# Performance work log

Hardware: AMD Instinct MI355X
Metric: run time of the kernel (lower is better)

## Reference

```python
import jax, jax.numpy as jnp
import numpy as np

# dims
B, L, HID = 4, 4096, 1024
H, D = 16, 64            # num_mem_heads, head_dim = HID // H
DM = 128                 # mem_intermediate = head_dim * mem_expansion_factor (2.0)
K = 4                    # conv_kernel
CS = 64                  # chunk_size
EPS = 1e-6


def setup_inputs() -> dict:
    key = jax.random.key(0)
    ks = jax.random.split(key, 16)
    std = 0.02
    f = lambda i, shape: jax.random.normal(ks[i], shape, jnp.float32) * std
    return {
        'hidden_states': jax.random.normal(ks[0], (B, L, HID), jnp.float32),
        'Wq': f(1, (HID, HID)), 'Wk': f(2, (HID, HID)), 'Wv': f(3, (HID, HID)),
        'conv_q_w': f(4, (HID, K)), 'conv_q_b': jnp.zeros((HID,), jnp.float32),
        'conv_k_w': f(5, (HID, K)), 'conv_k_b': jnp.zeros((HID,), jnp.float32),
        'conv_v_w': f(6, (HID, K)), 'conv_v_b': jnp.zeros((HID,), jnp.float32),
        'q_norm_w': jnp.ones((D,), jnp.float32), 'k_norm_w': jnp.ones((D,), jnp.float32),
        'mem_decay_w': f(7, (H, HID)), 'mem_decay_b': jnp.zeros((H,), jnp.float32),
        'surprise_w': f(8, (H, HID)), 'surprise_b': jnp.zeros((H,), jnp.float32),
        'lr_w': f(9, (H, HID)), 'lr_b': jnp.zeros((H,), jnp.float32),
        'W1': f(10, (H, D, DM)), 'W2': f(11, (H, DM, D)),
    }


def _silu_bwd(x):
    sig = jax.nn.sigmoid(x)
    return sig + jax.nn.silu(x) * (1.0 - sig)


def _rmsnorm(x, w):
    xf = x.astype(jnp.float32)
    var = jnp.mean(xf * xf, axis=-1, keepdims=True)
    return w * (xf * jax.lax.rsqrt(var + EPS)).astype(x.dtype)


def _causal_conv_silu(x, w, b):
    # x: [B, L, H, D] -> depthwise causal conv over time on C=H*D channels -> [B, H, L, D]
    Bs, Ls, Hh, Dd = x.shape
    xc = jnp.swapaxes(x.reshape(Bs, Ls, Hh * Dd), 1, 2)        # [B, C, L]
    xp = jnp.pad(xc, ((0, 0), (0, 0), (K - 1, 0)))             # left pad -> causal
    y = b[None, :, None]
    for k in range(K):
        y = y + w[None, :, k:k + 1] * xp[:, :, k:k + Ls]
    y = jax.nn.silu(y)
    return jnp.swapaxes(y.reshape(Bs, Hh, Dd, Ls), -2, -1)     # [B, H, L, D]


def _decayed_scan(d, v, init):
    # y_t = d_t * y_{t-1} + v_t, y_0 = init; d: [B,H,C,1], v: [B,H,C,dim], init: [B,H,1,dim]
    def comb(x, y):
        a1, b1 = x
        a2, b2 = y
        return a1 * a2, b1 * a2 + b2
    A, Bv = jax.lax.associative_scan(comb, (d, v), axis=2)
    return A * init + Bv


def _forward(hidden_states, Wq, Wk, Wv, conv_q_w, conv_q_b, conv_k_w, conv_k_b,
             conv_v_w, conv_v_b, q_norm_w, k_norm_w, mem_decay_w, mem_decay_b,
             surprise_w, surprise_b, lr_w, lr_b, W1, W2):
    x = hidden_states
    # projections -> [B, L, H, D]
    q = (x @ Wq.T).reshape(B, L, H, D)
    k = (x @ Wk.T).reshape(B, L, H, D)
    v = (x @ Wv.T).reshape(B, L, H, D)
    # depthwise causal conv + silu -> [B, H, L, D]
    q = _causal_conv_silu(q, conv_q_w, conv_q_b)
    k = _causal_conv_silu(k, conv_k_w, conv_k_b)
    v = _causal_conv_silu(v, conv_v_w, conv_v_b)
    # QK RMSNorm (per head_dim)
    q = _rmsnorm(q, q_norm_w)
    k = _rmsnorm(k, k_norm_w)
    # per-timestep gates -> [B, H, L, 1]
    mem_decay = 1.0 - jax.nn.sigmoid(x @ mem_decay_w.T + mem_decay_b)
    surprise_decay = jax.nn.sigmoid(x @ surprise_w.T + surprise_b)
    lr = jax.nn.sigmoid(x @ lr_w.T + lr_b)
    to_gate = lambda g: jnp.swapaxes(g, -2, -1)[..., None]
    mem_decay, surprise_decay, lr = to_gate(mem_decay), to_gate(surprise_decay), to_gate(lr)

    # split sequence into chunks: [N, B, H, CS, *]
    N = L // CS
    ch = lambda t: jnp.moveaxis(t.reshape(B, H, N, CS, t.shape[-1]), 2, 0)
    qs, ks_, vs = ch(q), ch(k), ch(v)
    mds, sds, lrs = ch(mem_decay), ch(surprise_decay), ch(lr)

    W1b = jnp.broadcast_to(W1[None], (B, H, D, DM))
    W2b = jnp.broadcast_to(W2[None], (B, H, DM, D))
    carry0 = (W1b, W2b,
              jnp.zeros((B, H, 1, DM), jnp.float32),   # W1_surprise
              jnp.zeros((B, H, 1, D), jnp.float32),    # W2_surprise
              jnp.zeros((B, H, 1, D), jnp.float32),    # key_momentum
              jnp.zeros((B, H, 1, DM), jnp.float32))   # X1_momentum

    def step(carry, inp):
        W1c, W2c, W1s, W2s, kmom, xmom = carry
        qc, kc, vc, md, sd, lrc = inp
        # memory MLP fwd with chunk-frozen weights
        Z1 = kc @ W1c                       # [B,H,CS,DM]
        X1 = jax.nn.silu(Z1)
        mems = X1 @ W2c                     # [B,H,CS,D]
        g_m = mems - vc
        g_Z1 = (g_m @ jnp.swapaxes(W2c, -2, -1)) * _silu_bwd(Z1)
        g_m = -lrc * g_m
        g_Z1 = -lrc * g_Z1
        # activation-space surprise/momentum scans (decayed linear recurrence)
        W1s_n = _decayed_scan(sd, g_Z1, W1s)[:, :, -1:, :]
        W2s_n = _decayed_scan(sd, g_m, W2s)[:, :, -1:, :]
        kmom_n = _decayed_scan(md, kc, kmom)[:, :, -1:, :]
        xmom_n = _decayed_scan(md, X1, xmom)[:, :, -1:, :]
        # weight update at chunk boundary: decay + outer-product of accumulated factors
        mprod = jnp.prod(md, axis=2, keepdims=True)          # [B,H,1,1]
        W1n = mprod * W1c + jnp.swapaxes(kmom_n, -2, -1) @ W1s_n
        W2n = mprod * W2c + jnp.swapaxes(xmom_n, -2, -1) @ W2s_n
        # retrieve with updated memory
        y = jax.nn.silu(qc @ W1n) @ W2n                      # [B,H,CS,D]
        return (W1n, W2n, W1s_n, W2s_n, kmom_n, xmom_n), y

    _, ys = jax.lax.scan(step, carry0, (qs, ks_, vs, mds, sds, lrs))
    mem_states = jnp.moveaxis(ys, 0, 2).reshape(B, H, L, D)
    # replicate torch: mem_states.transpose(-2,-1).reshape(B, L, H*D)
    return jnp.swapaxes(mem_states, -2, -1).reshape(B, L, H * D)


def reference(hidden_states, Wq, Wk, Wv, conv_q_w, conv_q_b, conv_k_w, conv_k_b,
              conv_v_w, conv_v_b, q_norm_w, k_norm_w, mem_decay_w, mem_decay_b,
              surprise_w, surprise_b, lr_w, lr_b, W1, W2):
    return _forward(hidden_states, Wq, Wk, Wv, conv_q_w, conv_q_b, conv_k_w, conv_k_b,
                    conv_v_w, conv_v_b, q_norm_w, k_norm_w, mem_decay_w, mem_decay_b,
                    surprise_w, surprise_b, lr_w, lr_b, W1, W2)
```

## Files before the change

kernel.cpp:

```cpp
#include <hip/hip_runtime.h>

#define B_ 4
#define L_ 4096
#define HID_ 1024
#define H_ 16
#define D_ 64
#define DM_ 128
#define CS_ 64
#define NCH_ 64
#define EPS_ 1e-6f

typedef __attribute__((ext_vector_type(8))) short bfrag_t;
typedef __attribute__((ext_vector_type(4))) float facc_t;

#define MFMA16(a,b,c) __builtin_amdgcn_mfma_f32_16x16x32_bf16(a,b,c,0,0,0)

__device__ __forceinline__ float sigf(float x){ return 1.0f/(1.0f + __expf(-x)); }

__device__ __forceinline__ unsigned f2bfu(float x){
  unsigned u = __float_as_uint(x);
  return (u + 0x7fffu + ((u>>16)&1u)) >> 16;
}
__device__ __forceinline__ float bf2f(unsigned short s){
  return __uint_as_float(((unsigned)s)<<16);
}
__device__ __forceinline__ unsigned cvtpk(float lo, float hi){
  unsigned r;
  asm("v_cvt_pk_bf16_f32 %0, %1, %2" : "=v"(r) : "v"(lo), "v"(hi));
  return r;
}
__device__ __forceinline__ float bflo(unsigned u){ return __uint_as_float(u<<16); }
__device__ __forceinline__ float bfhi(unsigned u){ return __uint_as_float(u & 0xffff0000u); }

__device__ __forceinline__ void gld16(const unsigned short* g, unsigned short* l){
  __builtin_amdgcn_global_load_lds(
      (const __attribute__((address_space(1))) unsigned int*)(const void*)g,
      (__attribute__((address_space(3))) unsigned int*)(void*)l,
      16, 0, 0);
}

#define DPP_ADD_(x, ctrl) x += __int_as_float(__builtin_amdgcn_update_dpp(0, __float_as_int(x), ctrl, 0xf, 0xf, true))
__device__ __forceinline__ float wsum64(float x){
  DPP_ADD_(x, 0x111);
  DPP_ADD_(x, 0x112);
  DPP_ADD_(x, 0x114);
  DPP_ADD_(x, 0x118);
  const float a = __int_as_float(__builtin_amdgcn_readlane(__float_as_int(x), 15));
  const float b = __int_as_float(__builtin_amdgcn_readlane(__float_as_int(x), 31));
  const float c = __int_as_float(__builtin_amdgcn_readlane(__float_as_int(x), 47));
  const float d = __int_as_float(__builtin_amdgcn_readlane(__float_as_int(x), 63));
  return (a+b)+(c+d);
}

__global__ __launch_bounds__(256) void cast_kernel(
    const float* __restrict__ x,  const float* __restrict__ wq,
    const float* __restrict__ wk, const float* __restrict__ wv,
    unsigned short* __restrict__ xb,  unsigned short* __restrict__ wqb,
    unsigned short* __restrict__ wkb, unsigned short* __restrict__ wvb)
{
  const int bid = blockIdx.x;
  const float* s; unsigned short* d; int base;
  if (bid < 16384){ s = x; d = xb; base = bid*1024; }
  else {
    int r = bid - 16384; const int a = r >> 10; r &= 1023; base = r*1024;
    s = (a==0)?wq:(a==1)?wk:wv;
    d = (a==0)?wqb:(a==1)?wkb:wvb;
  }
  const int i = base + threadIdx.x*4;
  float4 v = *(const float4*)(s + i);
  unsigned lo = f2bfu(v.x) | (f2bfu(v.y)<<16);
  unsigned hi = f2bfu(v.z) | (f2bfu(v.w)<<16);
  uint2 o; o.x = lo; o.y = hi;
  *(uint2*)(d + i) = o;
}

__global__ __launch_bounds__(256, 2) void gemm_bf16_nt(
    const unsigned short* __restrict__ A, const unsigned short* __restrict__ Bw,
    unsigned short* __restrict__ C, int M, int N, int K)
{
  __shared__ __align__(16) unsigned short As[2][4096];
  __shared__ __align__(16) unsigned short Bs[2][4096];
  const int tid = threadIdx.x;
  const int lane = tid & 63, wave = tid >> 6;
  const int lq = lane & 15, quad = lane >> 4;
  const int m0 = blockIdx.y*128, n0 = blockIdx.x*128;
  const int row = tid >> 2, ks = (tid & 3)*8;
  const int mo = (wave & 1)*64, no = (wave >> 1)*64;

  const unsigned short* pa0 = A  + (size_t)(m0 + row)*K + ks;
  const unsigned short* pa1 = pa0 + (size_t)64*K;
  const unsigned short* pb0 = Bw + (size_t)(n0 + row)*K + ks;
  const unsigned short* pb1 = pb0 + (size_t)64*K;

  facc_t acc[4][4];
  #pragma unroll
  for (int i=0;i<4;++i)
    #pragma unroll
    for (int j=0;j<4;++j) acc[i][j] = (facc_t){0.f,0.f,0.f,0.f};

  auto stage = [&](int buf, int kt){
    const int off = kt*32;
    unsigned short* ab = &As[buf][wave*512];
    unsigned short* bb = &Bs[buf][wave*512];
    gld16(pa0 + off, ab);
    gld16(pa1 + off, ab + 2048);
    gld16(pb0 + off, bb);
    gld16(pb1 + off, bb + 2048);
  };

  const int kiters = K >> 5;
  stage(0, 0);
  __syncthreads();

  int cur = 0;
  for (int kt = 0; kt < kiters; ++kt){
    if (kt+1 < kiters) stage(cur^1, kt+1);
    bfrag_t af[4], bf[4];
    #pragma unroll
    for (int mt=0;mt<4;++mt) af[mt] = *(const bfrag_t*)&As[cur][(mo+mt*16+lq)*32 + quad*8];
    #pragma unroll
    for (int nt=0;nt<4;++nt) bf[nt] = *(const bfrag_t*)&Bs[cur][(no+nt*16+lq)*32 + quad*8];
    #pragma unroll
    for (int mt=0;mt<4;++mt)
      #pragma unroll
      for (int nt=0;nt<4;++nt)
        acc[mt][nt] = MFMA16(af[mt], bf[nt], acc[mt][nt]);
    __syncthreads();
    cur ^= 1;
  }

  #pragma unroll
  for (int mt=0;mt<4;++mt)
    #pragma unroll
    for (int nt=0;nt<4;++nt)
      #pragma unroll
      for (int r=0;r<4;++r){
        const int rr = m0 + mo + mt*16 + quad*4 + r;
        const int cc = n0 + no + nt*16 + lq;
        const int t = cc >> 10, hh = (cc >> 6) & 15, dd = cc & 63;
        const int b = rr >> 12, l = rr & 4095;
        C[((((size_t)t*B_ + b)*H_ + hh)*L_ + l)*64 + dd]
            = (unsigned short)f2bfu(acc[mt][nt][r]);
      }
}

__global__ __launch_bounds__(256, 2) void gates_kernel(
  const float* __restrict__ x,
  const float* __restrict__ mdw, const float* __restrict__ mdb,
  const float* __restrict__ sw,  const float* __restrict__ sb,
  const float* __restrict__ lw,  const float* __restrict__ lb,
  float* __restrict__ cmb, float* __restrict__ c1b, float* __restrict__ ppb)
{
  __shared__ float xs[64][68];
  __shared__ float wg[48][68];
  const int tid = threadIdx.x;
  const int m0 = blockIdx.x * 64;
  const int tx = tid & 15, ty = tid >> 4;
  float acc[4][3];
  #pragma unroll
  for (int r=0;r<4;++r){ acc[r][0]=0.f; acc[r][1]=0.f; acc[r][2]=0.f; }

  for (int k0 = 0; k0 < HID_; k0 += 64){
    {
      const int r = tid >> 2, kq = tid & 3;
      const float* xp = x + (size_t)(m0 + r) * HID_ + k0 + kq*16;
      #pragma unroll
      for (int u=0;u<4;++u){
        float4 v = *(const float4*)(xp + u*4);
        *(float4*)&xs[r][kq*16 + u*4] = v;
      }
    }
    #pragma unroll
    for (int u=0;u<3;++u){
      const int idx = tid + 256*u;
      const int gi = idx >> 4, q = idx & 15;
      const float* wp = (gi < 16) ? (mdw + (size_t)gi*HID_)
                      : (gi < 32) ? (sw  + (size_t)(gi-16)*HID_)
                                  : (lw  + (size_t)(gi-32)*HID_);
      float4 v = *(const float4*)(wp + k0 + q*4);
      *(float4*)&wg[gi][q*4] = v;
    }
    __syncthreads();
    for (int kk=0; kk<64; ++kk){
      float xv[4], wv[3];
      #pragma unroll
      for (int r=0;r<4;++r) xv[r] = xs[ty*4+r][kk];
      #pragma unroll
      for (int gg=0;gg<3;++gg) wv[gg] = wg[tx*3+gg][kk];
      #pragma unroll
      for (int r=0;r<4;++r)
        #pragma unroll
        for (int gg=0;gg<3;++gg) acc[r][gg] += xv[r]*wv[gg];
    }
    __syncthreads();
  }

  float (*ls)[68] = xs;
  #pragma unroll
  for (int gg=0; gg<3; ++gg){
    const int gi = tx*3 + gg;
    const int s = gi >> 4, hh = gi & 15;
    const float bias = (s==0) ? mdb[hh] : (s==1) ? sb[hh] : lb[hh];
    #pragma unroll
    for (int r=0;r<4;++r) ls[gi][ty*4+r] = acc[r][gg] + bias;
  }
  __syncthreads();

  const int lane = tid & 63, wv2 = tid >> 6;
  const int b = m0 >> 12, n = (m0 & 4095) >> 6;
  #pragma unroll
  for (int u=0;u<4;++u){
    const int hh = wv2*4 + u;
    const float md = 1.0f - sigf(ls[hh][lane]);
    const float sd = sigf(ls[16+hh][lane]);
    const float lr = sigf(ls[32+hh][lane]);
    float vm = md, vs = sd;
    #pragma unroll
    for (int off = 1; off < 64; off <<= 1){
      float om = __shfl_down(vm, off);
      float os = __shfl_down(vs, off);
      if (lane + off < 64){ vm *= om; vs *= os; }
    }
    float mex = __shfl_down(vm, 1);
    float sex = __shfl_down(vs, 1);
    if (lane == 63){ mex = 1.0f; sex = 1.0f; }
    const size_t base = ((size_t)(b*16 + hh)*NCH_ + n)*64;
    cmb[base + lane] = mex;
    c1b[base + lane] = -lr * sex;
    if (lane == 0){
      ppb[((size_t)(b*16+hh)*NCH_ + n)*2 + 0] = vm;
      ppb[((size_t)(b*16+hh)*NCH_ + n)*2 + 1] = vs;
    }
  }
}

#define HALO_T_ ((size_t)64*64*3*64)

__global__ __launch_bounds__(192) void halo_kernel(
  const unsigned short* __restrict__ qg, const unsigned short* __restrict__ kg,
  const unsigned short* __restrict__ vg, unsigned short* __restrict__ halo)
{
  const int blk = blockIdx.x;
  const int bh = blk / 63;
  const int ch = blk % 63 + 1;
  const int tid = threadIdx.x;
  const int tt = tid >> 6, lane = tid & 63;
  const long src = ((long)bh*L_ + (long)ch*64 - 3 + tt)*64 + lane;
  const long dst = (((long)bh*64 + ch)*3 + tt)*64 + lane;
  halo[dst]               = qg[src];
  halo[dst +   HALO_T_]   = kg[src];
  halo[dst + 2*HALO_T_]   = vg[src];
}

__global__ __launch_bounds__(256) void prep_kernel(
  unsigned short* __restrict__ qg, unsigned short* __restrict__ kg,
  unsigned short* __restrict__ vg,
  const unsigned short* __restrict__ halo,
  const float* __restrict__ cmg,
  const float* __restrict__ cqw, const float* __restrict__ cqb,
  const float* __restrict__ ckw, const float* __restrict__ ckb,
  const float* __restrict__ cvw, const float* __restrict__ cvb,
  const float* __restrict__ qnw, const float* __restrict__ knw,
  float* __restrict__ kredg)
{
  const int blk = blockIdx.x;
  const int bh = blk >> 6, ch = blk & 63;
  const int tid = threadIdx.x;
  const int lane = tid & 63, wave = tid >> 6;
  const int h = bh & 15;
  const int c = h*64 + lane;

  float wq4[4], wk4[4], wv4[4];
  #pragma unroll
  for (int kk=0;kk<4;++kk){ wq4[kk]=cqw[c*4+kk]; wk4[kk]=ckw[c*4+kk]; wv4[kk]=cvw[c*4+kk]; }
  const float bq = cqb[c], bk = ckb[c], bv = cvb[c];
  const float qnf = qnw[lane], knf = knw[lane];

  const long base = ((long)bh*L_ + (long)ch*64)*64 + lane;
  const int r0 = wave*16;

  float qw_[3], kw_[3], vw_[3];
  #pragma unroll
  for (int t=0;t<3;++t){
    const int row = r0 - 3 + t;
    if (row >= 0){
      qw_[t] = bf2f(qg[base + (long)row*64]);
      kw_[t] = bf2f(kg[base + (long)row*64]);
      vw_[t] = bf2f(vg[base + (long)row*64]);
    } else if (ch == 0){
      qw_[t] = 0.f; kw_[t] = 0.f; vw_[t] = 0.f;
    } else {
      const long hb = (((long)bh*64 + ch)*3 + (row + 3))*64 + lane;
      qw_[t] = bf2f(halo[hb]);
      kw_[t] = bf2f(halo[hb +   HALO_T_]);
      vw_[t] = bf2f(halo[hb + 2*HALO_T_]);
    }
  }
  __syncthreads();

  const float* cmp = cmg + ((size_t)bh*NCH_ + ch)*64;
  float kp = 0.f;
  #pragma unroll 8
  for (int i=0;i<16;++i){
    const int row = r0 + i;
    const long a = base + (long)row*64;
    const float q0v = bf2f(qg[a]);
    const float k0v = bf2f(kg[a]);
    const float v0v = bf2f(vg[a]);
    float aq = bq + wq4[0]*qw_[0] + wq4[1]*qw_[1] + wq4[2]*qw_[2] + wq4[3]*q0v;
    float ak = bk + wk4[0]*kw_[0] + wk4[1]*kw_[1] + wk4[2]*kw_[2] + wk4[3]*k0v;
    float av = bv + wv4[0]*vw_[0] + wv4[1]*vw_[1] + wv4[2]*vw_[2] + wv4[3]*v0v;
    const float yk = ak*sigf(ak), yq = aq*sigf(aq), yv = av*sigf(av);
    const float ssk = wsum64(yk*yk);
    const float ssq = wsum64(yq*yq);
    const float vk = knf * yk * rsqrtf(ssk*(1.0f/64.0f) + EPS_);
    const float vq = qnf * yq * rsqrtf(ssq*(1.0f/64.0f) + EPS_);
    const unsigned short kb16 = (unsigned short)f2bfu(vk);
    qg[a] = (unsigned short)f2bfu(vq);
    kg[a] = kb16;
    vg[a] = (unsigned short)f2bfu(yv);
    kp += cmp[row] * bf2f(kb16);
    qw_[0]=qw_[1]; qw_[1]=qw_[2]; qw_[2]=q0v;
    kw_[0]=kw_[1]; kw_[1]=kw_[2]; kw_[2]=k0v;
    vw_[0]=vw_[1]; vw_[1]=vw_[2]; vw_[2]=v0v;
  }

  __shared__ float kpart[4][64];
  kpart[wave][lane] = kp;
  __syncthreads();
  if (wave == 0)
    kredg[((size_t)bh*NCH_ + ch)*64 + lane] =
        (kpart[0][lane]+kpart[1][lane]) + (kpart[2][lane]+kpart[3][lane]);
}

#define SK 72
#define SX 136

__global__ __launch_bounds__(1024, 4) void scan_kernel(
  const unsigned short* __restrict__ qg, const unsigned short* __restrict__ kg,
  const unsigned short* __restrict__ vg,
  const float* __restrict__ cmg, const float* __restrict__ c1g,
  const float* __restrict__ ppg, const float* __restrict__ krg,
  const float* __restrict__ W1in, const float* __restrict__ W2in,
  float* __restrict__ out)
{
  const int bh = blockIdx.x;
  const int h = bh & 15;
  const int tid = threadIdx.x;
  const int lane = tid & 63, wave = tid >> 6;
  const int lq = lane & 15, quad = lane >> 4;
  const int wg = wave & 3;
  const int rw = wg * 16;
  const int cw = wave >> 2;

  __shared__ __align__(16) unsigned short sm[63488];
  unsigned short* xbs = sm + 27648;
  unsigned short* W1T = sm + 36352;
  unsigned short* W2n = sm + 45568;
  unsigned short* W2T = sm + 54784;
  __shared__ float cmA[2][64], c1A[2][64], krA[2][64], ppS[2][2];
  __shared__ float kmomS[64], xmomS[128], w1momS[128], w2momS[64];
  __shared__ float xpart[4][128], w1part[4][128], w2part[4][64];

  {
    const int j = tid >> 3, q0 = (tid & 7) * 8;
    const float* w1p = W1in + (size_t)h * D_ * DM_;
    #pragma unroll
    for (int t=0;t<8;++t)
      W1T[j*SK + q0 + t] = (unsigned short)f2bfu(w1p[(size_t)(q0+t)*DM_ + j]);
    const float* w2p = W2in + (size_t)h * DM_ * D_ + (size_t)j*D_ + q0;
    #pragma unroll
    for (int t=0;t<8;++t){
      unsigned short v = (unsigned short)f2bfu(w2p[t]);
      W2n[j*SK + q0 + t] = v;
      W2T[(q0+t)*SX + j] = v;
    }
  }
  if (tid < 64){ kmomS[tid]=0.f; w2momS[tid]=0.f; }
  if (tid < 128){ xmomS[tid]=0.f; w1momS[tid]=0.f; }

  const long cbase = (long)bh * L_ * 64;
  const int tr = tid >> 4, tc = (tid & 15) * 4;

  uint2 rq2, rk2, rv2;
  float cmr=0.f, c1r=0.f, krr=0.f, ppr=0.f;

  auto stage_load = [&](int m){
    if (m >= NCH_) return;
    const long a = cbase + ((long)m*64 + tr)*64 + tc;
    rq2 = *(const uint2*)(qg + a);
    rk2 = *(const uint2*)(kg + a);
    rv2 = *(const uint2*)(vg + a);
    if (wave == 0){
      cmr = cmg[((size_t)bh*NCH_ + m)*64 + lane];
      c1r = c1g[((size_t)bh*NCH_ + m)*64 + lane];
      krr = krg[((size_t)bh*NCH_ + m)*64 + lane];
    }
    if (tid < 2) ppr = ppg[((size_t)bh*NCH_ + m)*2 + tid];
  };

  auto stage_store = [&](int m, int s){
    if (m >= NCH_) return;
    unsigned short* kc = sm + s*4608;
    unsigned short* qc = sm + 9216 + s*4608;
    unsigned short* gm = sm + 18432 + s*4608;
    *(uint2*)&kc[tr*SK + tc] = rk2;
    *(uint2*)&qc[tr*SK + tc] = rq2;
    *(uint2*)&gm[tr*SK + tc] = rv2;
    if (wave == 0){ cmA[s][lane] = cmr; c1A[s][lane] = c1r; krA[s][lane] = krr; }
    if (tid < 2) ppS[s][tid] = ppr;
  };

  stage_load(0);
  stage_store(0, 0);
  __syncthreads();

  for (int n = 0; n < NCH_; ++n){
    const int cur = n & 1, nxt = cur ^ 1;
    const unsigned short* kcs = sm + cur*4608;
    const unsigned short* qcs = sm + 9216 + cur*4608;
    unsigned short* gms = sm + 18432 + cur*4608;
    const int r0 = rw + quad*4;

    stage_load(n+1);

    facc_t zk[2];
    {
      const bfrag_t a0 = *(const bfrag_t*)&kcs[(rw+lq)*SK + quad*8];
      const bfrag_t a1 = *(const bfrag_t*)&kcs[(rw+lq)*SK + 32 + quad*8];
      const float4 cmv = *(const float4*)&cmA[cur][r0];
      #pragma unroll
      for (int nt=0;nt<2;++nt){
        const int j = cw*32 + nt*16 + lq;
        const bfrag_t b0 = *(const bfrag_t*)&W1T[j*SK + quad*8];
        const bfrag_t b1 = *(const bfrag_t*)&W1T[j*SK + 32 + quad*8];
        facc_t z = {0.f,0.f,0.f,0.f};
        z = MFMA16(a0,b0,z); z = MFMA16(a1,b1,z);
        zk[nt] = z;
        const float x0 = z[0]*sigf(z[0]), x1 = z[1]*sigf(z[1]);
        const float x2 = z[2]*sigf(z[2]), x3 = z[3]*sigf(z[3]);
        const unsigned p01 = cvtpk(x0,x1), p23 = cvtpk(x2,x3);
        xbs[(r0+0)*SX + j] = (unsigned short)p01;
        xbs[(r0+1)*SX + j] = (unsigned short)(p01>>16);
        xbs[(r0+2)*SX + j] = (unsigned short)p23;
        xbs[(r0+3)*SX + j] = (unsigned short)(p23>>16);
        float xp = cmv.x*x0 + cmv.y*x1 + cmv.z*x2 + cmv.w*x3;
        xp += __shfl_xor(xp, 16);
        xp += __shfl_xor(xp, 32);
        if (quad == 0) xpart[wg][j] = xp;
      }
    }
    __syncthreads();

    {
      bfrag_t xa[4];
      #pragma unroll
      for (int kt=0;kt<4;++kt) xa[kt] = *(const bfrag_t*)&xbs[(rw+lq)*SX + kt*32 + quad*8];
      const int e = cw*16 + lq;
      facc_t z = {0.f,0.f,0.f,0.f};
      #pragma unroll
      for (int kt=0;kt<4;++kt){
        const bfrag_t bb = *(const bfrag_t*)&W2T[e*SX + kt*32 + quad*8];
        z = MFMA16(xa[kt], bb, z);
      }
      const float g0 = z[0] - bf2f(gms[(r0+0)*SK + e]);
      const float g1 = z[1] - bf2f(gms[(r0+1)*SK + e]);
      const float g2 = z[2] - bf2f(gms[(r0+2)*SK + e]);
      const float g3 = z[3] - bf2f(gms[(r0+3)*SK + e]);
      const unsigned p01 = cvtpk(g0,g1), p23 = cvtpk(g2,g3);
      gms[(r0+0)*SK + e] = (unsigned short)p01;
      gms[(r0+1)*SK + e] = (unsigned short)(p01>>16);
      gms[(r0+2)*SK + e] = (unsigned short)p23;
      gms[(r0+3)*SK + e] = (unsigned short)(p23>>16);
      const float4 c1v = *(const float4*)&c1A[cur][r0];
      float wp = c1v.x*g0 + c1v.y*g1 + c1v.z*g2 + c1v.w*g3;
      wp += __shfl_xor(wp, 16);
      wp += __shfl_xor(wp, 32);
      if (quad == 0) w2part[wg][e] = wp;
    }
    if (tid < 64) kmomS[tid] = ppS[cur][0]*kmomS[tid] + krA[cur][tid];
    if (tid < 128)
      xmomS[tid] = ppS[cur][0]*xmomS[tid]
                 + ((xpart[0][tid]+xpart[1][tid])+(xpart[2][tid]+xpart[3][tid]));
    stage_store(n+1, nxt);
    __syncthreads();

    {
      const bfrag_t a0 = *(const bfrag_t*)&gms[(rw+lq)*SK + quad*8];
      const bfrag_t a1 = *(const bfrag_t*)&gms[(rw+lq)*SK + 32 + quad*8];
      const float4 c1v = *(const float4*)&c1A[cur][r0];
      #pragma unroll
      for (int nt=0;nt<2;++nt){
        const int j = cw*32 + nt*16 + lq;
        const bfrag_t b0 = *(const bfrag_t*)&W2n[j*SK + quad*8];
        const bfrag_t b1 = *(const bfrag_t*)&W2n[j*SK + 32 + quad*8];
        facc_t gz = {0.f,0.f,0.f,0.f};
        gz = MFMA16(a0,b0,gz); gz = MFMA16(a1,b1,gz);
        float d[4];
        #pragma unroll
        for (int r=0;r<4;++r){
          const float zz = zk[nt][r];
          const float sg = sigf(zz);
          d[r] = gz[r] * (sg * (1.0f + zz*(1.0f - sg)));
        }
        const unsigned p01 = cvtpk(d[0],d[1]), p23 = cvtpk(d[2],d[3]);
        xbs[(r0+0)*SX + j] = (unsigned short)p01;
        xbs[(r0+1)*SX + j] = (unsigned short)(p01>>16);
        xbs[(r0+2)*SX + j] = (unsigned short)p23;
        xbs[(r0+3)*SX + j] = (unsigned short)(p23>>16);
        float wp = c1v.x*d[0] + c1v.y*d[1] + c1v.z*d[2] + c1v.w*d[3];
        wp += __shfl_xor(wp, 16);
        wp += __shfl_xor(wp, 32);
        if (quad == 0) w1part[wg][j] = wp;
      }
    }
    if (tid < 64)
      w2momS[tid] = ppS[cur][1]*w2momS[tid]
                  + ((w2part[0][tid]+w2part[1][tid])+(w2part[2][tid]+w2part[3][tid]));
    __syncthreads();

    {
      const float Pmd = ppS[cur][0], Psd = ppS[cur][1];
      const int j = tid >> 3, q0 = (tid & 7)*8;
      const float w1m = Psd*w1momS[j]
          + ((w1part[0][j]+w1part[1][j])+(w1part[2][j]+w1part[3][j]));
      if ((tid & 7) == 0) w1momS[j] = w1m;
      const float xm = xmomS[j];
      const float4 km0 = *(const float4*)&kmomS[q0];
      const float4 km1 = *(const float4*)&kmomS[q0+4];
      {
        const int off = j*SK + q0;
        const uint4 w = *(const uint4*)&W1T[off];
        uint4 o;
        o.x = cvtpk(Pmd*bflo(w.x) + w1m*km0.x, Pmd*bfhi(w.x) + w1m*km0.y);
        o.y = cvtpk(Pmd*bflo(w.y) + w1m*km0.z, Pmd*bfhi(w.y) + w1m*km0.w);
        o.z = cvtpk(Pmd*bflo(w.z) + w1m*km1.x, Pmd*bfhi(w.z) + w1m*km1.y);
        o.w = cvtpk(Pmd*bflo(w.w) + w1m*km1.z, Pmd*bfhi(w.w) + w1m*km1.w);
        *(uint4*)&W1T[off] = o;
      }
      const float4 wm0 = *(const float4*)&w2momS[q0];
      const float4 wm1 = *(const float4*)&w2momS[q0+4];
      {
        const int off = j*SK + q0;
        const uint4 w = *(const uint4*)&W2n[off];
        uint4 o;
        o.x = cvtpk(Pmd*bflo(w.x) + xm*wm0.x, Pmd*bfhi(w.x) + xm*wm0.y);
        o.y = cvtpk(Pmd*bflo(w.y) + xm*wm0.z, Pmd*bfhi(w.y) + xm*wm0.w);
        o.z = cvtpk(Pmd*bflo(w.z) + xm*wm1.x, Pmd*bfhi(w.z) + xm*wm1.y);
        o.w = cvtpk(Pmd*bflo(w.w) + xm*wm1.z, Pmd*bfhi(w.w) + xm*wm1.w);
        *(uint4*)&W2n[off] = o;
      }
      const int e2 = tid >> 4, js = (tid & 15)*8;
      const float w2m = w2momS[e2];
      const float4 xm0 = *(const float4*)&xmomS[js];
      const float4 xm1 = *(const float4*)&xmomS[js+4];
      {
        const int off = e2*SX + js;
        const uint4 w = *(const uint4*)&W2T[off];
        uint4 o;
        o.x = cvtpk(Pmd*bflo(w.x) + xm0.x*w2m, Pmd*bfhi(w.x) + xm0.y*w2m);
        o.y = cvtpk(Pmd*bflo(w.y) + xm0.z*w2m, Pmd*bfhi(w.y) + xm0.w*w2m);
        o.z = cvtpk(Pmd*bflo(w.z) + xm1.x*w2m, Pmd*bfhi(w.z) + xm1.y*w2m);
        o.w = cvtpk(Pmd*bflo(w.w) + xm1.z*w2m, Pmd*bfhi(w.w) + xm1.w*w2m);
        *(uint4*)&W2T[off] = o;
      }
    }
    __syncthreads();

    {
      const bfrag_t a0 = *(const bfrag_t*)&qcs[(rw+lq)*SK + quad*8];
      const bfrag_t a1 = *(const bfrag_t*)&qcs[(rw+lq)*SK + 32 + quad*8];
      #pragma unroll
      for (int nt=0;nt<2;++nt){
        const int j = cw*32 + nt*16 + lq;
        const bfrag_t b0 = *(const bfrag_t*)&W1T[j*SK + quad*8];
        const bfrag_t b1 = *(const bfrag_t*)&W1T[j*SK + 32 + quad*8];
        facc_t z = {0.f,0.f,0.f,0.f};
        z = MFMA16(a0,b0,z); z = MFMA16(a1,b1,z);
        const float x0 = z[0]*sigf(z[0]), x1 = z[1]*sigf(z[1]);
        const float x2 = z[2]*sigf(z[2]), x3 = z[3]*sigf(z[3]);
        const unsigned p01 = cvtpk(x0,x1), p23 = cvtpk(x2,x3);
        xbs[(r0+0)*SX + j] = (unsigned short)p01;
        xbs[(r0+1)*SX + j] = (unsigned short)(p01>>16);
        xbs[(r0+2)*SX + j] = (unsigned short)p23;
        xbs[(r0+3)*SX + j] = (unsigned short)(p23>>16);
      }
    }
    __syncthreads();

    {
      bfrag_t xa[4];
      #pragma unroll
      for (int kt=0;kt<4;++kt) xa[kt] = *(const bfrag_t*)&xbs[(rw+lq)*SX + kt*32 + quad*8];
      const int e = cw*16 + lq;
      facc_t y = {0.f,0.f,0.f,0.f};
      #pragma unroll
      for (int kt=0;kt<4;++kt){
        const bfrag_t bb = *(const bfrag_t*)&W2T[e*SX + kt*32 + quad*8];
        y = MFMA16(xa[kt], bb, y);
      }
      float4 ov; ov.x = y[0]; ov.y = y[1]; ov.z = y[2]; ov.w = y[3];
      *(float4*)&out[(size_t)bh*D_*L_ + (size_t)e*L_ + n*64 + rw + quad*4] = ov;
    }
    __syncthreads();
  }
}

extern "C" void kernel_launch(void* const* d_in, const int* in_sizes, int n_in,
                              void* d_out, int out_size, void* d_ws, size_t ws_size,
                              hipStream_t stream)
{
  const float* x   = (const float*)d_in[0];
  const float* Wq  = (const float*)d_in[1];
  const float* Wk  = (const float*)d_in[2];
  const float* Wv  = (const float*)d_in[3];
  const float* cqw = (const float*)d_in[4];
  const float* cqb = (const float*)d_in[5];
  const float* ckw = (const float*)d_in[6];
  const float* ckb = (const float*)d_in[7];
  const float* cvw = (const float*)d_in[8];
  const float* cvb = (const float*)d_in[9];
  const float* qnw = (const float*)d_in[10];
  const float* knw = (const float*)d_in[11];
  const float* mdw = (const float*)d_in[12];
  const float* mdb = (const float*)d_in[13];
  const float* sw  = (const float*)d_in[14];
  const float* sb  = (const float*)d_in[15];
  const float* lw  = (const float*)d_in[16];
  const float* lb  = (const float*)d_in[17];
  const float* W1  = (const float*)d_in[18];
  const float* W2  = (const float*)d_in[19];
  float* out = (float*)d_out;

  const size_t SZ  = (size_t)B_ * L_ * HID_;
  const size_t WSZ = (size_t)HID_ * HID_;
  unsigned short* xb  = (unsigned short*)d_ws;
  unsigned short* wqb = xb  + SZ;
  unsigned short* wkb = wqb + WSZ;
  unsigned short* wvb = wkb + WSZ;
  unsigned short* qb  = wvb + WSZ;
  unsigned short* kb  = qb  + SZ;
  unsigned short* vb  = kb  + SZ;
  float* cmb = (float*)(vb + SZ);
  float* c1b = cmb + (size_t)B_*H_*NCH_*64;
  float* ppb = c1b + (size_t)B_*H_*NCH_*64;
  float* kredg = ppb + (size_t)B_*H_*NCH_*2;
  unsigned short* halo = (unsigned short*)(kredg + (size_t)B_*H_*NCH_*64);

  cast_kernel<<<16384 + 3*1024, 256, 0, stream>>>(x, Wq, Wk, Wv, xb, wqb, wkb, wvb);
  dim3 gg(3*HID_/128, (B_*L_)/128);
  gemm_bf16_nt<<<gg, 256, 0, stream>>>(xb, wqb, qb, B_*L_, 3*HID_, HID_);
  gates_kernel<<<(B_*L_)/64, 256, 0, stream>>>(x, mdw, mdb, sw, sb, lw, lb, cmb, c1b, ppb);
  halo_kernel<<<64*63, 192, 0, stream>>>(qb, kb, vb, halo);
  prep_kernel<<<B_*H_*NCH_, 256, 0, stream>>>(qb, kb, vb, halo, cmb,
                                              cqw, cqb, ckw, ckb, cvw, cvb,
                                              qnw, knw, kredg);
  scan_kernel<<<B_*H_, 1024, 0, stream>>>(qb, kb, vb, cmb, c1b, ppb, kredg,
                                          W1, W2, out);
}
```

Baseline: 772.6 us.

## Triple-buffer QKV GEMM loads and stage output through LDS for vector stores

The bf16 QKV projection GEMM moves from double to triple buffering, prefetching two k-tiles ahead. Each iteration waits on partial vmcnt counts with a raw barrier instead of a full __syncthreads drain. The epilogue writes accumulators into a padded LDS tile, then issues coalesced 16-byte stores into the head-split layout, replacing scattered 2-byte stores. Launch bounds are raised to 3 blocks per CU. LDS use grows to 48KB per block, and the hand-written waitcnt logic depends on the async gld16 loads being counted by vmcnt.

```diff
diff --git a/kernel.cpp b/kernel.cpp
--- a/kernel.cpp
+++ b/kernel.cpp
@@ -74,12 +74,16 @@
   *(uint2*)(d + i) = o;
 }
 
-__global__ __launch_bounds__(256, 2) void gemm_bf16_nt(
+#define SC_ 132
+
+__global__ __launch_bounds__(256, 3) void gemm_bf16_nt(
     const unsigned short* __restrict__ A, const unsigned short* __restrict__ Bw,
     unsigned short* __restrict__ C, int M, int N, int K)
 {
-  __shared__ __align__(16) unsigned short As[2][4096];
-  __shared__ __align__(16) unsigned short Bs[2][4096];
+  __shared__ __align__(16) unsigned short smem[24576];
+  unsigned short* As = smem;
+  unsigned short* Bs = smem + 12288;
+
   const int tid = threadIdx.x;
   const int lane = tid & 63, wave = tid >> 6;
   const int lq = lane & 15, quad = lane >> 4;
@@ -100,8 +104,8 @@
 
   auto stage = [&](int buf, int kt){
     const int off = kt*32;
-    unsigned short* ab = &As[buf][wave*512];
-    unsigned short* bb = &Bs[buf][wave*512];
+    unsigned short* ab = As + buf*4096 + wave*512;
+    unsigned short* bb = Bs + buf*4096 + wave*512;
     gld16(pa0 + off, ab);
     gld16(pa1 + off, ab + 2048);
     gld16(pb0 + off, bb);
@@ -110,38 +114,64 @@
 
   const int kiters = K >> 5;
   stage(0, 0);
-  __syncthreads();
+  stage(1, 1);
+  asm volatile("s_waitcnt vmcnt(4)" ::: "memory");
+  __builtin_amdgcn_s_barrier();
+  __builtin_amdgcn_sched_barrier(0);
 
   int cur = 0;
   for (int kt = 0; kt < kiters; ++kt){
-    if (kt+1 < kiters) stage(cur^1, kt+1);
+    if (kt+2 < kiters){
+      int b2 = cur + 2; if (b2 >= 3) b2 -= 3;
+      stage(b2, kt+2);
+    }
+    const unsigned short* as = As + cur*4096;
+    const unsigned short* bs = Bs + cur*4096;
     bfrag_t af[4], bf[4];
     #pragma unroll
-    for (int mt=0;mt<4;++mt) af[mt] = *(const bfrag_t*)&As[cur][(mo+mt*16+lq)*32 + quad*8];
-    #pragma unroll
-    for (int nt=0;nt<4;++nt) bf[nt] = *(const bfrag_t*)&Bs[cur][(no+nt*16+lq)*32 + quad*8];
+    for (int mt=0;mt<4;++mt) af[mt] = *(const bfrag_t*)&as[(mo+mt*16+lq)*32 + quad*8];
+    #pragma unroll
+    for (int nt=0;nt<4;++nt) bf[nt] = *(const bfrag_t*)&bs[(no+nt*16+lq)*32 + quad*8];
     #pragma unroll
     for (int mt=0;mt<4;++mt)
       #pragma unroll
       for (int nt=0;nt<4;++nt)
         acc[mt][nt] = MFMA16(af[mt], bf[nt], acc[mt][nt]);
-    __syncthreads();
-    cur ^= 1;
-  }
-
+    if (kt+1 < kiters){
+      if (kt+2 < kiters) asm volatile("s_waitcnt vmcnt(4)" ::: "memory");
+      else               asm volatile("s_waitcnt vmcnt(0)" ::: "memory");
+      __builtin_amdgcn_s_barrier();
+      __builtin_amdgcn_sched_barrier(0);
+    }
+    cur = (cur == 2) ? 0 : cur + 1;
+  }
+
+  __syncthreads();
+  unsigned short* Cs = smem;
   #pragma unroll
   for (int mt=0;mt<4;++mt)
     #pragma unroll
     for (int nt=0;nt<4;++nt)
       #pragma unroll
       for (int r=0;r<4;++r){
-        const int rr = m0 + mo + mt*16 + quad*4 + r;
-        const int cc = n0 + no + nt*16 + lq;
-        const int t = cc >> 10, hh = (cc >> 6) & 15, dd = cc & 63;
-        const int b = rr >> 12, l = rr & 4095;
-        C[((((size_t)t*B_ + b)*H_ + hh)*L_ + l)*64 + dd]
-            = (unsigned short)f2bfu(acc[mt][nt][r]);
-      }
+        const int lr = mo + mt*16 + quad*4 + r;
+        const int lc = no + nt*16 + lq;
+        Cs[lr*SC_ + lc] = (unsigned short)f2bfu(acc[mt][nt][r]);
+      }
+  __syncthreads();
+  #pragma unroll
+  for (int u=0;u<8;++u){
+    const int idx = tid + 256*u;
+    const int ml = idx >> 4, s = idx & 15;
+    const int rr = m0 + ml;
+    const int cc0 = n0 + s*8;
+    const int t = cc0 >> 10, hh = (cc0 >> 6) & 15, dd0 = cc0 & 63;
+    const int b = rr >> 12, l = rr & 4095;
+    uint2 v0 = *(const uint2*)&Cs[ml*SC_ + s*8];
+    uint2 v1 = *(const uint2*)&Cs[ml*SC_ + s*8 + 4];
+    uint4 v; v.x = v0.x; v.y = v0.y; v.z = v1.x; v.w = v1.y;
+    *(uint4*)&C[((((size_t)t*B_ + b)*H_ + hh)*L_ + l)*64 + dd0] = v;
+  }
 }
 
 __global__ __launch_bounds__(256, 2) void gates_kernel(
@@ -352,6 +382,7 @@
   const int wg = wave & 3;
   const int rw = wg * 16;
   const int cw = wave >> 2;
+  const int r0 = rw + quad*4;
 
   __shared__ __align__(16) unsigned short sm[63488];
   unsigned short* xbs = sm + 27648;
@@ -420,7 +451,6 @@
     const unsigned short* kcs = sm + cur*4608;
     const unsigned short* qcs = sm + 9216 + cur*4608;
     unsigned short* gms = sm + 18432 + cur*4608;
-    const int r0 = rw + quad*4;
 
     stage_load(n+1);
 
```

Result: no change. 767.4 us (-0.7%).
